# Kernel optimization log

Hardware: AMD Instinct MI355X
Metric: run time of the kernel (lower is better)

## Reference

```python
import jax, jax.numpy as jnp
import numpy as np

KAPPA = 0.5


def setup_inputs() -> dict:
    key = jax.random.key(0)
    embeddings = jax.random.normal(key, (8, 4096, 64), dtype=jnp.float32)
    return {"embeddings": embeddings}


def reference(embeddings):
    # logits[b, n, m] = kappa * <emb[b,n], emb[b,m]>   -> [B, N, N]
    logits = KAPPA * jnp.einsum("bnd,bmd->bnm", embeddings, embeddings)
    B = logits.shape[0]
    # logsumexp over both matrix dims, per batch element
    loss = jax.scipy.special.logsumexp(logits.reshape(B, -1), axis=1)
    return loss.mean()
```

## Files before the change

kernel.cpp:

```cpp
#include <hip/hip_runtime.h>
#include <math.h>

#define BATCH 8
#define NTOK  4096
#define DIM   64
#define BM    128
#define NT    (NTOK / BM)
#define TPB   (NT * (NT + 1) / 2)
#define TOTAL (BATCH * TPB)
#define KAPPA 0.5f
#define LOG2E 1.4426950408889634f
#define LN2   0.6931471805599453f
#define M2FIX 48.0f

typedef _Float16 f16x8 __attribute__((ext_vector_type(8)));
typedef float    f32x16 __attribute__((ext_vector_type(16)));

__device__ __forceinline__ float EXP2(float x) {
#if __has_builtin(__builtin_amdgcn_exp2f)
    return __builtin_amdgcn_exp2f(x);
#else
    return __expf(x * LN2);
#endif
}

__global__ __launch_bounds__(256)
void conv_f16(const float* __restrict__ emb, f16x8* __restrict__ o16) {
    const size_t i = (size_t)blockIdx.x * 256 + threadIdx.x;
    const float4 v0 = *(const float4*)(emb + i * 8);
    const float4 v1 = *(const float4*)(emb + i * 8 + 4);
    f16x8 p;
    p[0] = (_Float16)v0.x; p[1] = (_Float16)v0.y;
    p[2] = (_Float16)v0.z; p[3] = (_Float16)v0.w;
    p[4] = (_Float16)v1.x; p[5] = (_Float16)v1.y;
    p[6] = (_Float16)v1.z; p[7] = (_Float16)v1.w;
    o16[i] = p;
}

__global__ __launch_bounds__(256, 5)
void gram_lse_partial(const f16x8* __restrict__ w16, float* __restrict__ ws) {
    __shared__ f16x8 S[2048];

    const int tid  = threadIdx.x;
    const int lane = tid & 63;
    const int w    = tid >> 6;
    const int p    = blockIdx.x;
    const int bb   = (p & 7) * TPB + (p >> 3);
    const int b    = bb / TPB;
    int t = bb - b * TPB;
    int ti = 0;
    while (t >= NT - ti) { t -= NT - ti; ++ti; }
    const int tj = ti + t;

    const char* pA16 = (const char*)(w16 + ((size_t)b * NTOK + (size_t)ti * BM) * 8);
    const char* pB16 = (const char*)(w16 + ((size_t)b * NTOK + (size_t)tj * BM) * 8);

    {
        const char* pbase  = (w < 2) ? pA16 : pB16;
        const int   upBase = (w & 1) * 512 + lane;
#pragma unroll
        for (int q = 0; q < 8; ++q) {
            const int up  = upBase + q * 64;
            const int g   = up >> 7;
            const int rp  = up & 127;
            const int off = (((rp ^ g) << 7) | (g << 4));
            __builtin_amdgcn_global_load_lds(
                (const __attribute__((address_space(1))) void*)(pbase + off),
                (__attribute__((address_space(3))) void*)&S[(size_t)w * 512 + q * 64],
                16, 0, 0);
        }
    }
    __syncthreads();

    const int half = lane >> 5;
    const int ln31 = lane & 31;
    const int waveR = (w & 1) * 64;
    const int waveC = (w >> 1) * 64;
    const float c2 = KAPPA * LOG2E;

    float s0 = 0.f, s1 = 0.f, s2 = 0.f, s3 = 0.f;
#pragma unroll 1
    for (int q = 0; q < 4; ++q) {
        const int ra = waveR + (q >> 1) * 32 + ln31;
        const int rb = waveC + (q & 1) * 32 + ln31;
        f32x16 acc = {};
#pragma unroll
        for (int s = 0; s < 4; ++s) {
            const int g = 2 * s + half;
            acc = __builtin_amdgcn_mfma_f32_32x32x16_f16(
                S[g * BM + (ra ^ g)], S[1024 + g * BM + (rb ^ g)], acc, 0, 0, 0);
        }
#pragma unroll
        for (int e = 0; e < 16; e += 4) {
            s0 += EXP2(fmaf(c2, acc[e],     -M2FIX));
            s1 += EXP2(fmaf(c2, acc[e + 1], -M2FIX));
            s2 += EXP2(fmaf(c2, acc[e + 2], -M2FIX));
            s3 += EXP2(fmaf(c2, acc[e + 3], -M2FIX));
        }
    }
    float lsum = (s0 + s1) + (s2 + s3);
#pragma unroll
    for (int off = 32; off > 0; off >>= 1)
        lsum += __shfl_xor(lsum, off);

    if (lane == 0) {
        const float wgt = (ti == tj) ? 1.f : 2.f;
        ws[4 * (size_t)bb + w] = wgt * lsum;
    }
}

__global__ __launch_bounds__(512)
void reduce_lse(const float* __restrict__ ws, float* __restrict__ out) {
    const int tid  = threadIdx.x;
    const int w    = tid >> 6;
    const int lane = tid & 63;
    __shared__ float lse8[BATCH];

    const float* p = ws + (size_t)w * TPB * 4;
    float s = 0.f;
#pragma unroll
    for (int c = 0; c < 33; ++c) s += p[lane + 64 * c];
#pragma unroll
    for (int off = 32; off > 0; off >>= 1) s += __shfl_xor(s, off);

    if (lane == 0) lse8[w] = LN2 * (M2FIX + log2f(s));
    __syncthreads();
    if (tid == 0) {
        float a = 0.f;
        for (int i = 0; i < BATCH; ++i) a += lse8[i];
        out[0] = a * (1.f / BATCH);
    }
}

extern "C" void kernel_launch(void* const* d_in, const int* in_sizes, int n_in,
                              void* d_out, int out_size, void* d_ws, size_t ws_size,
                              hipStream_t stream) {
    const float* emb = (const float*)d_in[0];
    float* out = (float*)d_out;
    f16x8* w16 = (f16x8*)d_ws;
    float* prt = (float*)((char*)d_ws + (4u << 20));

    conv_f16<<<NTOK * BATCH * DIM / 8 / 256, 256, 0, stream>>>(emb, w16);
    gram_lse_partial<<<TOTAL, 256, 0, stream>>>(w16, prt);
    reduce_lse<<<1, 512, 0, stream>>>(prt, out);
}
```

Measured before the change: 79.83 us.

## Load MFMA fragments directly to registers and fold scale into fp16 conversion

The conversion kernel now pre-multiplies embeddings by sqrt(kappa*log2e). The MFMA output can then go straight into exp2, with no fma and no fixed max offset. The Gram kernel drops LDS staging and its barrier: each wave loads its A/B fragments directly from global memory into registers, and the four 32x32 sub-tiles are fully unrolled. Occupancy hint lowers from 5 to 4 blocks. Risks are redundant global/L2 traffic across waves, and overflow headroom now depends on the unshifted exp2 sum staying within fp32 range.

Result: slower. 91.17 us (+14.2%).

```diff
diff --git a/kernel.cpp b/kernel.cpp
--- a/kernel.cpp
+++ b/kernel.cpp
@@ -11,7 +11,7 @@
 #define KAPPA 0.5f
 #define LOG2E 1.4426950408889634f
 #define LN2   0.6931471805599453f
-#define M2FIX 48.0f
+#define SQRTC2 0.8493218f
 
 typedef _Float16 f16x8 __attribute__((ext_vector_type(8)));
 typedef float    f32x16 __attribute__((ext_vector_type(16)));
@@ -30,17 +30,15 @@
     const float4 v0 = *(const float4*)(emb + i * 8);
     const float4 v1 = *(const float4*)(emb + i * 8 + 4);
     f16x8 p;
-    p[0] = (_Float16)v0.x; p[1] = (_Float16)v0.y;
-    p[2] = (_Float16)v0.z; p[3] = (_Float16)v0.w;
-    p[4] = (_Float16)v1.x; p[5] = (_Float16)v1.y;
-    p[6] = (_Float16)v1.z; p[7] = (_Float16)v1.w;
+    p[0] = (_Float16)(v0.x * SQRTC2); p[1] = (_Float16)(v0.y * SQRTC2);
+    p[2] = (_Float16)(v0.z * SQRTC2); p[3] = (_Float16)(v0.w * SQRTC2);
+    p[4] = (_Float16)(v1.x * SQRTC2); p[5] = (_Float16)(v1.y * SQRTC2);
+    p[6] = (_Float16)(v1.z * SQRTC2); p[7] = (_Float16)(v1.w * SQRTC2);
     o16[i] = p;
 }
 
-__global__ __launch_bounds__(256, 5)
+__global__ __launch_bounds__(256, 4)
 void gram_lse_partial(const f16x8* __restrict__ w16, float* __restrict__ ws) {
-    __shared__ f16x8 S[2048];
-
     const int tid  = threadIdx.x;
     const int lane = tid & 63;
     const int w    = tid >> 6;
@@ -52,52 +50,70 @@
     while (t >= NT - ti) { t -= NT - ti; ++ti; }
     const int tj = ti + t;
 
-    const char* pA16 = (const char*)(w16 + ((size_t)b * NTOK + (size_t)ti * BM) * 8);
-    const char* pB16 = (const char*)(w16 + ((size_t)b * NTOK + (size_t)tj * BM) * 8);
-
-    {
-        const char* pbase  = (w < 2) ? pA16 : pB16;
-        const int   upBase = (w & 1) * 512 + lane;
-#pragma unroll
-        for (int q = 0; q < 8; ++q) {
-            const int up  = upBase + q * 64;
-            const int g   = up >> 7;
-            const int rp  = up & 127;
-            const int off = (((rp ^ g) << 7) | (g << 4));
-            __builtin_amdgcn_global_load_lds(
-                (const __attribute__((address_space(1))) void*)(pbase + off),
-                (__attribute__((address_space(3))) void*)&S[(size_t)w * 512 + q * 64],
-                16, 0, 0);
-        }
-    }
-    __syncthreads();
+    const f16x8* pA = w16 + ((size_t)b * NTOK + (size_t)ti * BM) * 8;
+    const f16x8* pB = w16 + ((size_t)b * NTOK + (size_t)tj * BM) * 8;
 
     const int half = lane >> 5;
     const int ln31 = lane & 31;
-    const int waveR = (w & 1) * 64;
-    const int waveC = (w >> 1) * 64;
-    const float c2 = KAPPA * LOG2E;
+    const int rA = (w & 1) * 64 + ln31;
+    const int rB = (w >> 1) * 64 + ln31;
+
+    f16x8 aL[4], aH[4], bL[4], bH[4];
+#pragma unroll
+    for (int s = 0; s < 4; ++s) {
+        const int g = 2 * s + half;
+        aL[s] = pA[rA * 8 + g];
+        aH[s] = pA[(rA + 32) * 8 + g];
+        bL[s] = pB[rB * 8 + g];
+        bH[s] = pB[(rB + 32) * 8 + g];
+    }
 
     float s0 = 0.f, s1 = 0.f, s2 = 0.f, s3 = 0.f;
-#pragma unroll 1
-    for (int q = 0; q < 4; ++q) {
-        const int ra = waveR + (q >> 1) * 32 + ln31;
-        const int rb = waveC + (q & 1) * 32 + ln31;
+    {
         f32x16 acc = {};
 #pragma unroll
-        for (int s = 0; s < 4; ++s) {
-            const int g = 2 * s + half;
-            acc = __builtin_amdgcn_mfma_f32_32x32x16_f16(
-                S[g * BM + (ra ^ g)], S[1024 + g * BM + (rb ^ g)], acc, 0, 0, 0);
-        }
+        for (int s = 0; s < 4; ++s)
+            acc = __builtin_amdgcn_mfma_f32_32x32x16_f16(aL[s], bL[s], acc, 0, 0, 0);
 #pragma unroll
         for (int e = 0; e < 16; e += 4) {
-            s0 += EXP2(fmaf(c2, acc[e],     -M2FIX));
-            s1 += EXP2(fmaf(c2, acc[e + 1], -M2FIX));
-            s2 += EXP2(fmaf(c2, acc[e + 2], -M2FIX));
-            s3 += EXP2(fmaf(c2, acc[e + 3], -M2FIX));
+            s0 += EXP2(acc[e]);     s1 += EXP2(acc[e + 1]);
+            s2 += EXP2(acc[e + 2]); s3 += EXP2(acc[e + 3]);
         }
     }
+    {
+        f32x16 acc = {};
+#pragma unroll
+        for (int s = 0; s < 4; ++s)
+            acc = __builtin_amdgcn_mfma_f32_32x32x16_f16(aL[s], bH[s], acc, 0, 0, 0);
+#pragma unroll
+        for (int e = 0; e < 16; e += 4) {
+            s0 += EXP2(acc[e]);     s1 += EXP2(acc[e + 1]);
+            s2 += EXP2(acc[e + 2]); s3 += EXP2(acc[e + 3]);
+        }
+    }
+    {
+        f32x16 acc = {};
+#pragma unroll
+        for (int s = 0; s < 4; ++s)
+            acc = __builtin_amdgcn_mfma_f32_32x32x16_f16(aH[s], bL[s], acc, 0, 0, 0);
+#pragma unroll
+        for (int e = 0; e < 16; e += 4) {
+            s0 += EXP2(acc[e]);     s1 += EXP2(acc[e + 1]);
+            s2 += EXP2(acc[e + 2]); s3 += EXP2(acc[e + 3]);
+        }
+    }
+    {
+        f32x16 acc = {};
+#pragma unroll
+        for (int s = 0; s < 4; ++s)
+            acc = __builtin_amdgcn_mfma_f32_32x32x16_f16(aH[s], bH[s], acc, 0, 0, 0);
+#pragma unroll
+        for (int e = 0; e < 16; e += 4) {
+            s0 += EXP2(acc[e]);     s1 += EXP2(acc[e + 1]);
+            s2 += EXP2(acc[e + 2]); s3 += EXP2(acc[e + 3]);
+        }
+    }
+
     float lsum = (s0 + s1) + (s2 + s3);
 #pragma unroll
     for (int off = 32; off > 0; off >>= 1)
@@ -123,7 +139,7 @@
 #pragma unroll
     for (int off = 32; off > 0; off >>= 1) s += __shfl_xor(s, off);
 
-    if (lane == 0) lse8[w] = LN2 * (M2FIX + log2f(s));
+    if (lane == 0) lse8[w] = LN2 * log2f(s);
     __syncthreads();
     if (tid == 0) {
         float a = 0.f;
```
